# Optimization experiments

Measured on AMD Instinct MI355X. Metric: run time of the kernel, lower is better.

Reference implementation:

```python
import jax, jax.numpy as jnp
import numpy as np

B, S, E, H, W = 4, 2048, 1024, 16, 128
HD = E // H

def setup_inputs() -> dict:
    key = jax.random.key(0)
    ks = jax.random.split(key, 5)
    scale = 1.0 / np.sqrt(E)
    x = jax.random.normal(ks[0], (B, S, E), dtype=jnp.float32)
    w_in = jax.random.uniform(ks[1], (3 * E, E), dtype=jnp.float32, minval=-scale, maxval=scale)
    b_in = jnp.zeros((3 * E,), dtype=jnp.float32)
    w_out = jax.random.uniform(ks[2], (E, E), dtype=jnp.float32, minval=-scale, maxval=scale)
    b_out = jnp.zeros((E,), dtype=jnp.float32)
    return {"x": x, "w_in": w_in, "b_in": b_in, "w_out": w_out, "b_out": b_out}

def reference(x, w_in, b_in, w_out, b_out):
    b, s, e = x.shape
    # fused QKV projection (torch MultiheadAttention in_proj)
    qkv = x @ w_in.T + b_in                      # [B,S,3E]
    q, k, v = jnp.split(qkv, 3, axis=-1)
    q = q.reshape(b, s, H, HD).transpose(0, 2, 1, 3)  # [B,H,S,HD]
    k = k.reshape(b, s, H, HD).transpose(0, 2, 1, 3)
    v = v.reshape(b, s, H, HD).transpose(0, 2, 1, 3)
    scores = jnp.einsum('bhqd,bhkd->bhqk', q, k) / jnp.sqrt(jnp.asarray(HD, x.dtype))
    # banded causal mask: row i attends to columns [i-W, i]
    i = jnp.arange(s)[:, None]
    j = jnp.arange(s)[None, :]
    allowed = (j <= i) & (j >= i - W)            # [S,S]
    scores = jnp.where(allowed[None, None], scores, jnp.asarray(-1e9, x.dtype))
    attn = jax.nn.softmax(scores, axis=-1)
    out = jnp.einsum('bhqk,bhkd->bhqd', attn, v)  # [B,H,S,HD]
    out = out.transpose(0, 2, 1, 3).reshape(b, s, e)
    return out @ w_out.T + b_out
```

## Files before the change

### kernel.cpp

```cpp
#include <hip/hip_runtime.h>
#include <stdint.h>

#define SLEN 2048
#define EMB  1024
#define NHEAD 16
#define HDIM  64
#define WINSZ 128

typedef __attribute__((ext_vector_type(8))) __bf16 bf16x8;
typedef __attribute__((ext_vector_type(4))) float  f32x4;

__device__ __forceinline__ unsigned short f2bf(float f) {
  union { float f; unsigned int u; } v;
  v.f = f;
  unsigned int r = v.u + 0x7FFFu + ((v.u >> 16) & 1u);
  return (unsigned short)(r >> 16);
}

__device__ __forceinline__ unsigned int pack_bf(float a, float b) {
  union { float f; unsigned int u; } x, y;
  x.f = a; y.f = b;
  return ((y.u + 0x8000u) & 0xFFFF0000u) | ((x.u + 0x8000u) >> 16);
}

__global__ void cvt_all(const float* __restrict__ x,
                        const float* __restrict__ wi,
                        const float* __restrict__ wo,
                        unsigned short* __restrict__ dst) {
  const long n0 = 8388608, n1 = n0 + 3145728, n2 = n1 + 1048576;
  long i = ((long)blockIdx.x * 256 + threadIdx.x) * 4;
  if (i >= n2) return;
  const float* src; long off;
  if (i < n0)      { src = x;  off = i; }
  else if (i < n1) { src = wi; off = i - n0; }
  else             { src = wo; off = i - n1; }
  float4 f = *(const float4*)(src + off);
  ushort4 o;
  o.x = f2bf(f.x); o.y = f2bf(f.y); o.z = f2bf(f.z); o.w = f2bf(f.w);
  *(ushort4*)(dst + i) = o;
}

#define AS1(p) (const __attribute__((address_space(1))) unsigned int*)((const void*)(p))
#define AS3(p) (__attribute__((address_space(3))) unsigned int*)((void*)(p))

template <int MODE>
__global__ __launch_bounds__(512, 2) void gemm_nt(
    const unsigned short* __restrict__ A,
    const unsigned short* __restrict__ B,
    const float* __restrict__ bias,
    void* __restrict__ Cout,
    unsigned short* __restrict__ vt,
    int M, int N, int K, int ldc)
{
  __shared__ unsigned short lds[73728];
  const int tid  = threadIdx.x;
  const int wave = tid >> 6, lane = tid & 63;
  const int quad = lane >> 4, l16 = lane & 15;
  const int wm = (wave >> 2) * 64, wn = (wave & 3) * 64;
  const int swz = l16 & 7;

  const int nwgx = gridDim.x;
  const int nwg  = nwgx * gridDim.y;
  const int orig = blockIdx.y * nwgx + blockIdx.x;
  const int bswz = (orig & 7) * (nwg >> 3) + (orig >> 3);
  const long mBase = (long)(bswz / nwgx) * 128;
  const long nBase = (long)(bswz % nwgx) * 256;

  const int lr  = lane >> 3;
  const int lks = ((lane & 7) ^ lr) * 8;
  const unsigned short* Abase = A + (mBase + lr) * (long)K + lks;
  const unsigned short* Bbase = B + (nBase + lr) * (long)K + lks;

#define STAGE3(TT, dstOff, H) do {                                                     \
    const long _kc = (long)(TT) * 64;                                                  \
    const int _ar = wave * 16 + (H) * 8;                                               \
    const int _br = wave * 32 + (H) * 16;                                              \
    __builtin_amdgcn_global_load_lds(AS1(Abase + (long)_ar * K + _kc),                 \
                                     AS3(lds + (dstOff) + _ar * 64), 16, 0, 0);        \
    __builtin_amdgcn_global_load_lds(AS1(Bbase + (long)_br * K + _kc),                 \
                                     AS3(lds + (dstOff) + 8192 + _br * 64), 16, 0, 0); \
    __builtin_amdgcn_global_load_lds(AS1(Bbase + (long)(_br + 8) * K + _kc),           \
                                     AS3(lds + (dstOff) + 8192 + (_br + 8) * 64), 16, 0, 0); \
  } while (0)

  f32x4 acc[4][4];
#pragma unroll
  for (int i = 0; i < 4; ++i)
#pragma unroll
    for (int j = 0; j < 4; ++j)
#pragma unroll
      for (int r = 0; r < 4; ++r) acc[i][j][r] = 0.f;

  const int NT = K >> 6;

  STAGE3(0, 0, 0); STAGE3(0, 0, 1);
  STAGE3(1, 24576, 0); STAGE3(1, 24576, 1);

  int curOff = 0, stgOff = 49152;
  for (int T = 0; T < NT; ++T) {
    if (T + 1 < NT) asm volatile("s_waitcnt vmcnt(6)" ::: "memory");
    else            asm volatile("s_waitcnt vmcnt(0)" ::: "memory");
    __builtin_amdgcn_s_barrier();
    __builtin_amdgcn_sched_barrier(0);

    const unsigned short* Ar = lds + curOff;
    const unsigned short* Br = lds + curOff + 8192;
    const bool doStage = (T + 2 < NT);

#pragma unroll
    for (int s = 0; s < 2; ++s) {
      bf16x8 aF[4], bF[4];
#pragma unroll
      for (int i = 0; i < 4; ++i)
        aF[i] = *(const bf16x8*)(Ar + (wm + i * 16 + l16) * 64 + (((s * 4 + quad) ^ swz) * 8));
#pragma unroll
      for (int j = 0; j < 4; ++j)
        bF[j] = *(const bf16x8*)(Br + (wn + j * 16 + l16) * 64 + (((s * 4 + quad) ^ swz) * 8));
      if (doStage) STAGE3(T + 2, stgOff, s);
      asm volatile("s_waitcnt lgkmcnt(0)" ::: "memory");
      __builtin_amdgcn_sched_barrier(0);
      __builtin_amdgcn_s_setprio(1);
#pragma unroll
      for (int i = 0; i < 4; ++i)
#pragma unroll
        for (int j = 0; j < 4; ++j)
          acc[i][j] = __builtin_amdgcn_mfma_f32_16x16x32_bf16(aF[i], bF[j], acc[i][j], 0, 0, 0);
      __builtin_amdgcn_s_setprio(0);
    }
    curOff = (curOff == 49152) ? 0 : curOff + 24576;
    stgOff = (stgOff == 49152) ? 0 : stgOff + 24576;
  }
#undef STAGE3

  if (MODE == 1 && nBase >= 2048) {
#pragma unroll
    for (int j = 0; j < 4; ++j) {
      const int nG = (int)nBase + wn + j * 16 + l16;
      const float bv = bias[nG];
      const int hd = nG - 2048;
      const int hh = hd >> 6, dd = hd & 63;
#pragma unroll
      for (int i = 0; i < 4; ++i) {
        const int mG0 = (int)mBase + wm + i * 16 + quad * 4;
        const int bb = mG0 >> 11, ss = mG0 & 2047;
        ushort4 o;
        o.x = f2bf(acc[i][j][0] + bv);
        o.y = f2bf(acc[i][j][1] + bv);
        o.z = f2bf(acc[i][j][2] + bv);
        o.w = f2bf(acc[i][j][3] + bv);
        *(ushort4*)(vt + (((long)(bb * NHEAD + hh)) * HDIM + dd) * SLEN + ss) = o;
      }
    }
  } else {
#pragma unroll
    for (int j = 0; j < 4; ++j) {
      const long nG = nBase + wn + j * 16 + l16;
      const float bv = bias[nG];
#pragma unroll
      for (int i = 0; i < 4; ++i)
#pragma unroll
        for (int r = 0; r < 4; ++r) {
          const long mG = mBase + wm + i * 16 + quad * 4 + r;
          const float v = acc[i][j][r] + bv;
          if (MODE == 1) ((unsigned short*)Cout)[mG * ldc + nG] = f2bf(v);
          else           ((float*)Cout)[mG * ldc + nG] = v;
        }
    }
  }
}

__global__ __launch_bounds__(512, 4) void local_attn(
    const unsigned short* __restrict__ qk,
    const unsigned short* __restrict__ vT,
    unsigned short* __restrict__ outw)
{
  const int qb = blockIdx.x;
  const int h  = blockIdx.y;
  const int b  = blockIdx.z;
  const int tid = threadIdx.x;
  const int wave = tid >> 6, lane = tid & 63;
  const int quad = lane >> 4, l16 = lane & 15;

  __shared__ unsigned short Klds[256 * 64];
  __shared__ unsigned short Vlds[64 * 256];

  const int kwin0 = qb * 128 - WINSZ;

  {
    const int kr = lane >> 3, kc = lane & 7;
    const long colOff = 1024 + h * HDIM + ((kc ^ kr) * 8);
#pragma unroll
    for (int t = 0; t < 4; ++t) {
      const int u = wave * 4 + t;
      const int sk = max(kwin0 + u * 8 + kr, 0);
      const unsigned short* g = qk + (long)(b * SLEN + sk) * 2048 + colOff;
      __builtin_amdgcn_global_load_lds(AS1(g), AS3(Klds + u * 512), 16, 0, 0);
    }
  }
  {
    const unsigned short* vbase = vT + ((long)(b * NHEAD + h)) * HDIM * SLEN;
#pragma unroll
    for (int t = 0; t < 4; ++t) {
      const int c = t * 512 + tid;
      const int d = c >> 5, k8 = c & 31;
      const int s0 = max(kwin0 + k8 * 8, 0);
      uint4 v = *(const uint4*)(vbase + (long)d * SLEN + s0);
      *(uint4*)(Vlds + d * 256 + ((k8 ^ (d & 7)) * 8)) = v;
    }
  }

  const int q0 = qb * 128 + wave * 16;
  const long qrow = (long)(b * SLEN + q0 + l16) * 2048 + h * HDIM;
  const bf16x8 qB0 = *(const bf16x8*)(qk + qrow + quad * 8);
  const bf16x8 qB1 = *(const bf16x8*)(qk + qrow + 32 + quad * 8);

  __syncthreads();

  const int lbase = (wave * 16) & ~31;
  const int kx = l16 & 7;
  const int a0 = (quad ^ kx) * 8;
  const int a1 = ((4 + quad) ^ kx) * 8;
  f32x4 sc[5][2];
#pragma unroll
  for (int it = 0; it < 5; ++it) {
    const int l0 = lbase + it * 32;
#pragma unroll
    for (int half = 0; half < 2; ++half) {
      const unsigned short* kr_ = Klds + (l0 + half * 16 + l16) * 64;
      const bf16x8 kA0 = *(const bf16x8*)(kr_ + a0);
      const bf16x8 kA1 = *(const bf16x8*)(kr_ + a1);
      f32x4 s;
#pragma unroll
      for (int r = 0; r < 4; ++r) s[r] = 0.f;
      s = __builtin_amdgcn_mfma_f32_16x16x32_bf16(kA0, qB0, s, 0, 0, 0);
      s = __builtin_amdgcn_mfma_f32_16x16x32_bf16(kA1, qB1, s, 0, 0, 0);
      sc[it][half] = s;
    }
  }

  const int qlocal = WINSZ + wave * 16 + l16;
  const int lo = max(wave * 16 + l16, kwin0 < 0 ? -kwin0 : 0);
  const int kb = lbase + quad * 4;
  float m = -3.0e38f;
#pragma unroll
  for (int it = 0; it < 5; ++it)
#pragma unroll
    for (int half = 0; half < 2; ++half)
#pragma unroll
      for (int r = 0; r < 4; ++r) {
        const int kl = kb + it * 32 + half * 16 + r;
        float v = sc[it][half][r] * 0.125f;
        v = (kl >= lo && kl <= qlocal) ? v : -3.0e38f;
        sc[it][half][r] = v;
        m = fmaxf(m, v);
      }
  m = fmaxf(m, __shfl_xor(m, 16, 64));
  m = fmaxf(m, __shfl_xor(m, 32, 64));

  float lsum = 0.f;
#pragma unroll
  for (int it = 0; it < 5; ++it)
#pragma unroll
    for (int half = 0; half < 2; ++half)
#pragma unroll
      for (int r = 0; r < 4; ++r) {
        const float e = __expf(sc[it][half][r] - m);
        sc[it][half][r] = e;
        lsum += e;
      }
  lsum += __shfl_xor(lsum, 16, 64);
  lsum += __shfl_xor(lsum, 32, 64);
  const float invl = 1.0f / lsum;

  f32x4 Oacc[4];
#pragma unroll
  for (int dt = 0; dt < 4; ++dt)
#pragma unroll
    for (int r = 0; r < 4; ++r) Oacc[dt][r] = 0.f;

#pragma unroll
  for (int it = 0; it < 5; ++it) {
    const int l0 = lbase + it * 32;
    const unsigned int u0 = pack_bf(sc[it][0][0], sc[it][0][1]);
    const unsigned int u1 = pack_bf(sc[it][0][2], sc[it][0][3]);
    const unsigned int u2 = pack_bf(sc[it][1][0], sc[it][1][1]);
    const unsigned int u3 = pack_bf(sc[it][1][2], sc[it][1][3]);
    unsigned int breg[4];
#pragma unroll
    for (int r = 0; r < 4; ++r) {
      const int srcl = ((quad & 1) * 2 + (r >> 1)) * 16 + l16;
      const unsigned int ga = __shfl((int)((r & 1) ? u1 : u0), srcl, 64);
      const unsigned int gb = __shfl((int)((r & 1) ? u3 : u2), srcl, 64);
      breg[r] = (quad >> 1) ? gb : ga;
    }
    union { unsigned int u[4]; bf16x8 v; } pB;
    pB.u[0] = breg[0]; pB.u[1] = breg[1]; pB.u[2] = breg[2]; pB.u[3] = breg[3];

    const int chBase = (l0 >> 3);
#pragma unroll
    for (int dt = 0; dt < 4; ++dt) {
      const int ch = (chBase + quad) ^ kx;
      const bf16x8 vA = *(const bf16x8*)(Vlds + (dt * 16 + l16) * 256 + ch * 8);
      Oacc[dt] = __builtin_amdgcn_mfma_f32_16x16x32_bf16(vA, pB.v, Oacc[dt], 0, 0, 0);
    }
  }

  const long obase = (long)(b * SLEN + q0 + l16) * EMB + h * HDIM;
#pragma unroll
  for (int dt = 0; dt < 4; ++dt) {
    ushort4 o;
    o.x = f2bf(Oacc[dt][0] * invl);
    o.y = f2bf(Oacc[dt][1] * invl);
    o.z = f2bf(Oacc[dt][2] * invl);
    o.w = f2bf(Oacc[dt][3] * invl);
    *(ushort4*)(outw + obase + dt * 16 + quad * 4) = o;
  }
}

extern "C" void kernel_launch(void* const* d_in, const int* in_sizes, int n_in,
                              void* d_out, int out_size, void* d_ws, size_t ws_size,
                              hipStream_t stream) {
  const float* x     = (const float*)d_in[0];
  const float* w_in  = (const float*)d_in[1];
  const float* b_in  = (const float*)d_in[2];
  const float* w_out = (const float*)d_in[3];
  const float* b_out = (const float*)d_in[4];
  float* out = (float*)d_out;

  char* ws = (char*)d_ws;
  unsigned short* xb    = (unsigned short*)(ws + 0);
  unsigned short* winb  = (unsigned short*)(ws + 16777216);
  unsigned short* woutb = (unsigned short*)(ws + 23068672);
  unsigned short* qkb   = (unsigned short*)(ws + 25165824);
  unsigned short* attn  = (unsigned short*)(ws + 58720256);
  unsigned short* vT    = (unsigned short*)(ws + 75497472);

  const long ncv = 8388608 + 3145728 + 1048576;
  cvt_all<<<(int)(ncv / 1024), 256, 0, stream>>>(x, w_in, w_out, xb);

  gemm_nt<1><<<dim3(3072 / 256, 8192 / 128), 512, 0, stream>>>(
      xb, winb, b_in, (void*)qkb, vT, 8192, 3072, 1024, 2048);

  local_attn<<<dim3(SLEN / 128, NHEAD, 4), 512, 0, stream>>>(qkb, vT, attn);

  gemm_nt<0><<<dim3(1024 / 256, 8192 / 128), 512, 0, stream>>>(
      attn, woutb, b_out, (void*)out, nullptr, 8192, 1024, 1024, 1024);
}
```

Before: 203.3 us.

## Enlarge GEMM tile to 256x256 with five-slot half-tile LDS ring pipeline

The bf16 GEMM block tile grows from 128x256 to 256x256, with each wave computing 128x64 (8x4 MFMA tiles), which halves the grid and raises operand reuse per global load. The LDS staging becomes a five-slot ring of 128-row half-tiles, refilled in quarter steps interleaved with the MFMA phases and separated by extra barriers. This cuts global and L2 traffic per FLOP. In exchange it doubles accumulator registers, adds LDS usage and barriers, and leaves fewer workgroups, which hurts occupancy and load balance on the smaller output-projection GEMM (128 blocks).

```diff
diff --git a/kernel.cpp b/kernel.cpp
--- a/kernel.cpp
+++ b/kernel.cpp
@@ -52,18 +52,22 @@
     unsigned short* __restrict__ vt,
     int M, int N, int K, int ldc)
 {
-  __shared__ unsigned short lds[73728];
+  __shared__ unsigned short lds[81920];
   const int tid  = threadIdx.x;
   const int wave = tid >> 6, lane = tid & 63;
   const int quad = lane >> 4, l16 = lane & 15;
-  const int wm = (wave >> 2) * 64, wn = (wave & 3) * 64;
+  const int wm2 = (wave >> 2) * 128;
+  const int wn2 = (wave & 3) * 64;
+  const int ah  = wave >> 2;
+  const int bh  = (wave & 3) >> 1;
+  const int brow = (wave & 1) * 64;
   const int swz = l16 & 7;
 
   const int nwgx = gridDim.x;
   const int nwg  = nwgx * gridDim.y;
   const int orig = blockIdx.y * nwgx + blockIdx.x;
   const int bswz = (orig & 7) * (nwg >> 3) + (orig >> 3);
-  const long mBase = (long)(bswz / nwgx) * 128;
+  const long mBase = (long)(bswz / nwgx) * 256;
   const long nBase = (long)(bswz % nwgx) * 256;
 
   const int lr  = lane >> 3;
@@ -71,77 +75,96 @@
   const unsigned short* Abase = A + (mBase + lr) * (long)K + lks;
   const unsigned short* Bbase = B + (nBase + lr) * (long)K + lks;
 
-#define STAGE3(TT, dstOff, H) do {                                                     \
-    const long _kc = (long)(TT) * 64;                                                  \
-    const int _ar = wave * 16 + (H) * 8;                                               \
-    const int _br = wave * 32 + (H) * 16;                                              \
-    __builtin_amdgcn_global_load_lds(AS1(Abase + (long)_ar * K + _kc),                 \
-                                     AS3(lds + (dstOff) + _ar * 64), 16, 0, 0);        \
-    __builtin_amdgcn_global_load_lds(AS1(Bbase + (long)_br * K + _kc),                 \
-                                     AS3(lds + (dstOff) + 8192 + _br * 64), 16, 0, 0); \
-    __builtin_amdgcn_global_load_lds(AS1(Bbase + (long)(_br + 8) * K + _kc),           \
-                                     AS3(lds + (dstOff) + 8192 + (_br + 8) * 64), 16, 0, 0); \
+  const int NT = K >> 6;
+
+#define STAGE_PART(HH, SL, P) do {                                                   \
+    if ((HH) < 2 * NT) {                                                             \
+      const int _r = wave * 16 + ((P) & 1) * 8;                                      \
+      const long _off = ((long)(((HH) & 1) * 128 + _r)) * K + (long)((HH) >> 1) * 64;\
+      if ((P) < 2)                                                                   \
+        __builtin_amdgcn_global_load_lds(AS1(Abase + _off),                          \
+            AS3(lds + (SL) * 16384 + _r * 64), 16, 0, 0);                            \
+      else                                                                           \
+        __builtin_amdgcn_global_load_lds(AS1(Bbase + _off),                          \
+            AS3(lds + (SL) * 16384 + 8192 + _r * 64), 16, 0, 0);                     \
+    }                                                                                \
   } while (0)
 
-  f32x4 acc[4][4];
-#pragma unroll
-  for (int i = 0; i < 4; ++i)
+  f32x4 acc[8][4];
+#pragma unroll
+  for (int i = 0; i < 8; ++i)
 #pragma unroll
     for (int j = 0; j < 4; ++j)
 #pragma unroll
       for (int r = 0; r < 4; ++r) acc[i][j][r] = 0.f;
 
-  const int NT = K >> 6;
-
-  STAGE3(0, 0, 0); STAGE3(0, 0, 1);
-  STAGE3(1, 24576, 0); STAGE3(1, 24576, 1);
-
-  int curOff = 0, stgOff = 49152;
+#pragma unroll
+  for (int h = 0; h < 3; ++h) {
+    STAGE_PART(h, h, 0); STAGE_PART(h, h, 1);
+    STAGE_PART(h, h, 2); STAGE_PART(h, h, 3);
+  }
+  asm volatile("s_waitcnt vmcnt(4)" ::: "memory");
+  __builtin_amdgcn_s_barrier();
+
+  int slA = ah, slB = bh;
+  int s3 = 3, s4 = 4;
   for (int T = 0; T < NT; ++T) {
-    if (T + 1 < NT) asm volatile("s_waitcnt vmcnt(6)" ::: "memory");
-    else            asm volatile("s_waitcnt vmcnt(0)" ::: "memory");
-    __builtin_amdgcn_s_barrier();
-    __builtin_amdgcn_sched_barrier(0);
-
-    const unsigned short* Ar = lds + curOff;
-    const unsigned short* Br = lds + curOff + 8192;
-    const bool doStage = (T + 2 < NT);
-
-#pragma unroll
-    for (int s = 0; s < 2; ++s) {
-      bf16x8 aF[4], bF[4];
-#pragma unroll
-      for (int i = 0; i < 4; ++i)
-        aF[i] = *(const bf16x8*)(Ar + (wm + i * 16 + l16) * 64 + (((s * 4 + quad) ^ swz) * 8));
-#pragma unroll
-      for (int j = 0; j < 4; ++j)
-        bF[j] = *(const bf16x8*)(Br + (wn + j * 16 + l16) * 64 + (((s * 4 + quad) ^ swz) * 8));
-      if (doStage) STAGE3(T + 2, stgOff, s);
+    const unsigned short* Ar = lds + slA * 16384;
+    const unsigned short* Br = lds + slB * 16384 + 8192 + brow * 64;
+    bf16x8 bF[4];
+#pragma unroll
+    for (int q = 0; q < 4; ++q) {
+      const int s = q >> 1, mh = q & 1;
+      if (mh == 0) {
+#pragma unroll
+        for (int j = 0; j < 4; ++j)
+          bF[j] = *(const bf16x8*)(Br + (j * 16 + l16) * 64 + (((s * 4 + quad) ^ swz) * 8));
+      }
+      bf16x8 aF[4];
+#pragma unroll
+      for (int t = 0; t < 4; ++t)
+        aF[t] = *(const bf16x8*)(Ar + ((mh * 4 + t) * 16 + l16) * 64 + (((s * 4 + quad) ^ swz) * 8));
+
+      {
+        const int hh = 2 * T + 3 + s;
+        const int sl = s ? s4 : s3;
+        STAGE_PART(hh, sl, mh * 2);
+        STAGE_PART(hh, sl, mh * 2 + 1);
+      }
+      if (q == 3) {
+        if (T == NT - 2)     asm volatile("s_waitcnt vmcnt(0)" ::: "memory");
+        else if (T < NT - 2) asm volatile("s_waitcnt vmcnt(4)" ::: "memory");
+      }
+      __builtin_amdgcn_s_barrier();
       asm volatile("s_waitcnt lgkmcnt(0)" ::: "memory");
       __builtin_amdgcn_sched_barrier(0);
       __builtin_amdgcn_s_setprio(1);
 #pragma unroll
-      for (int i = 0; i < 4; ++i)
+      for (int t = 0; t < 4; ++t)
 #pragma unroll
         for (int j = 0; j < 4; ++j)
-          acc[i][j] = __builtin_amdgcn_mfma_f32_16x16x32_bf16(aF[i], bF[j], acc[i][j], 0, 0, 0);
+          acc[mh * 4 + t][j] =
+              __builtin_amdgcn_mfma_f32_16x16x32_bf16(aF[t], bF[j], acc[mh * 4 + t][j], 0, 0, 0);
       __builtin_amdgcn_s_setprio(0);
-    }
-    curOff = (curOff == 49152) ? 0 : curOff + 24576;
-    stgOff = (stgOff == 49152) ? 0 : stgOff + 24576;
-  }
-#undef STAGE3
+      __builtin_amdgcn_s_barrier();
+    }
+    slA += 2; if (slA >= 5) slA -= 5;
+    slB += 2; if (slB >= 5) slB -= 5;
+    s3  += 2; if (s3  >= 5) s3  -= 5;
+    s4  += 2; if (s4  >= 5) s4  -= 5;
+  }
+#undef STAGE_PART
 
   if (MODE == 1 && nBase >= 2048) {
 #pragma unroll
     for (int j = 0; j < 4; ++j) {
-      const int nG = (int)nBase + wn + j * 16 + l16;
+      const int nG = (int)nBase + wn2 + j * 16 + l16;
       const float bv = bias[nG];
       const int hd = nG - 2048;
       const int hh = hd >> 6, dd = hd & 63;
 #pragma unroll
-      for (int i = 0; i < 4; ++i) {
-        const int mG0 = (int)mBase + wm + i * 16 + quad * 4;
+      for (int i = 0; i < 8; ++i) {
+        const int mG0 = (int)mBase + wm2 + i * 16 + quad * 4;
         const int bb = mG0 >> 11, ss = mG0 & 2047;
         ushort4 o;
         o.x = f2bf(acc[i][j][0] + bv);
@@ -154,13 +177,13 @@
   } else {
 #pragma unroll
     for (int j = 0; j < 4; ++j) {
-      const long nG = nBase + wn + j * 16 + l16;
+      const long nG = nBase + wn2 + j * 16 + l16;
       const float bv = bias[nG];
 #pragma unroll
-      for (int i = 0; i < 4; ++i)
+      for (int i = 0; i < 8; ++i)
 #pragma unroll
         for (int r = 0; r < 4; ++r) {
-          const long mG = mBase + wm + i * 16 + quad * 4 + r;
+          const long mG = mBase + wm2 + i * 16 + quad * 4 + r;
           const float v = acc[i][j][r] + bv;
           if (MODE == 1) ((unsigned short*)Cout)[mG * ldc + nG] = f2bf(v);
           else           ((float*)Cout)[mG * ldc + nG] = v;
@@ -338,11 +361,11 @@
   const long ncv = 8388608 + 3145728 + 1048576;
   cvt_all<<<(int)(ncv / 1024), 256, 0, stream>>>(x, w_in, w_out, xb);
 
-  gemm_nt<1><<<dim3(3072 / 256, 8192 / 128), 512, 0, stream>>>(
+  gemm_nt<1><<<dim3(3072 / 256, 8192 / 256), 512, 0, stream>>>(
       xb, winb, b_in, (void*)qkb, vT, 8192, 3072, 1024, 2048);
 
   local_attn<<<dim3(SLEN / 128, NHEAD, 4), 512, 0, stream>>>(qkb, vT, attn);
 
-  gemm_nt<0><<<dim3(1024 / 256, 8192 / 128), 512, 0, stream>>>(
+  gemm_nt<0><<<dim3(1024 / 256, 8192 / 256), 512, 0, stream>>>(
       attn, woutb, b_out, (void*)out, nullptr, 8192, 1024, 1024, 1024);
 }
```

New measurement: 224.1 us. +10.2%, slower.
